# Kernel tuning notes

Measured on AMD Instinct MI355X. Metric: run time of the kernel, lower is better.

The kernel has to match this reference:

```python
import jax, jax.numpy as jnp
import numpy as np

NUM_ITERS = 20  # fixed in the original forward: transcribe(dna, iterations=20)


def transcribe(dna_seed, dna_a, dna_b):
    """Fractal DNA decompression: 20 elementwise contractive-map iterations
    over the full weight tensor, starting from the DNA seed."""
    def step(w, ab):
        a, b = ab
        w = a * w + b * jnp.sin(w)
        return w, None
    w, _ = jax.lax.scan(step, dna_seed, (dna_a, dna_b))
    return w  # [out_features, in_features]


def setup_inputs() -> dict:
    key = jax.random.key(0)
    k1, k2, k3, k4, k5 = jax.random.split(key, 5)
    TOKENS, IN_F, OUT_F = 2048, 4096, 4096
    return {
        "x": jax.random.normal(k1, (TOKENS, IN_F), dtype=jnp.float32),
        "dna_seed": jax.random.normal(k2, (OUT_F, IN_F), dtype=jnp.float32),
        "dna_a": jax.random.uniform(k3, (NUM_ITERS,), dtype=jnp.float32),
        "dna_b": jax.random.uniform(k4, (NUM_ITERS,), dtype=jnp.float32),
        "bias": jax.random.normal(k5, (OUT_F,), dtype=jnp.float32),
    }


def reference(x, dna_seed, dna_a, dna_b, bias):
    weight = transcribe(dna_seed, dna_a, dna_b)          # [out, in]
    # F.linear(x, weight, bias) == x @ weight.T + bias
    return jnp.einsum('ti,oi->to', x, weight) + bias     # [tokens, out]
```

## Files before the change

### kernel.cpp

```cpp
#include <hip/hip_runtime.h>

typedef __attribute__((ext_vector_type(8))) short short8;
typedef __attribute__((ext_vector_type(4))) float floatx4;

#define TOKENS 2048
#define IN_F   4096
#define OUT_F  4096
#define NITER  20

#define INV_2PI 0.15915494309189535f
#define TWO_PI  6.283185307179586f

__device__ __forceinline__ unsigned short f2bf(float f) {
    unsigned int u = __builtin_bit_cast(unsigned int, f);
    u += 0x7fffu + ((u >> 16) & 1u);
    return (unsigned short)(u >> 16);
}

__device__ __forceinline__ void step4(float4& v, float a, float bc) {
    v.x = __builtin_fmaf(bc, __builtin_amdgcn_sinf(v.x), a * v.x);
    v.y = __builtin_fmaf(bc, __builtin_amdgcn_sinf(v.y), a * v.y);
    v.z = __builtin_fmaf(bc, __builtin_amdgcn_sinf(v.z), a * v.z);
    v.w = __builtin_fmaf(bc, __builtin_amdgcn_sinf(v.w), a * v.w);
}

#define WBLOCKS (OUT_F * IN_F / 8 / 256)
#define XBLOCKS (TOKENS * IN_F / 8 / 256)

__global__ __launch_bounds__(256) void transcribe_fused_kernel(
    const float4* __restrict__ seed, const float4* __restrict__ xin,
    const float* __restrict__ da, const float* __restrict__ db,
    short8* __restrict__ w_out, short8* __restrict__ x_out)
{
    const int b = blockIdx.x;
    short8 o;
    if (b < WBLOCKS) {
        int i = b * 256 + threadIdx.x;
        float4 u = seed[2 * i];
        float4 v = seed[2 * i + 1];
        u.x *= INV_2PI; u.y *= INV_2PI; u.z *= INV_2PI; u.w *= INV_2PI;
        v.x *= INV_2PI; v.y *= INV_2PI; v.z *= INV_2PI; v.w *= INV_2PI;
#pragma unroll
        for (int t = 0; t < NITER; t++) {
            float a = da[t], bc = db[t] * INV_2PI;
            step4(u, a, bc);
            step4(v, a, bc);
        }
        o[0] = (short)f2bf(u.x * TWO_PI); o[1] = (short)f2bf(u.y * TWO_PI);
        o[2] = (short)f2bf(u.z * TWO_PI); o[3] = (short)f2bf(u.w * TWO_PI);
        o[4] = (short)f2bf(v.x * TWO_PI); o[5] = (short)f2bf(v.y * TWO_PI);
        o[6] = (short)f2bf(v.z * TWO_PI); o[7] = (short)f2bf(v.w * TWO_PI);
        w_out[i] = o;
    } else {
        int i = (b - WBLOCKS) * 256 + threadIdx.x;
        float4 u = xin[2 * i];
        float4 v = xin[2 * i + 1];
        o[0] = (short)f2bf(u.x); o[1] = (short)f2bf(u.y);
        o[2] = (short)f2bf(u.z); o[3] = (short)f2bf(u.w);
        o[4] = (short)f2bf(v.x); o[5] = (short)f2bf(v.y);
        o[6] = (short)f2bf(v.z); o[7] = (short)f2bf(v.w);
        x_out[i] = o;
    }
}

__device__ __forceinline__ void g2l16(const ushort* g, ushort* l) {
    __builtin_amdgcn_global_load_lds(
        (const __attribute__((address_space(1))) unsigned int*)g,
        (__attribute__((address_space(3))) unsigned int*)l, 16, 0, 0);
}

#define BK     64
#define BM     256
#define BN     128
#define NT     (IN_F / BK)
#define ASLOT  (BM * BK)
#define BSLOT  (BN * BK)
#define LDS_BYTES (3 * (ASLOT + BSLOT) * 2)

__global__ __launch_bounds__(512, 2) void gemm_bt_kernel(
    const ushort* __restrict__ A,
    const ushort* __restrict__ B,
    const float* __restrict__ bias,
    float* __restrict__ C)
{
    extern __shared__ ushort lds[];
    ushort* As = lds;
    ushort* Bs = lds + 3 * ASLOT;

    const int tid  = threadIdx.x;
    const int lane = tid & 63;
    const int wid  = tid >> 6;
    const int g    = wid >> 2;
    const int w2   = wid & 3;
    const int wm   = (w2 >> 1) << 7;
    const int wn   = (w2 & 1) << 6;
    const int fm   = lane & 15;
    const int q    = lane >> 4;

    const int bid = blockIdx.x;
    const int jj  = bid >> 3;
    const int bn  = (bid & 7) * 4 + (jj & 3);
    const int bm  = jj >> 2;

    const int gcol = (((lane & 7) ^ (lane >> 3)) << 3);

    const ushort* gA = A + (size_t)(bm * BM) * IN_F;
    const ushort* gB = B + (size_t)(bn * BN) * IN_F;

    floatx4 acc[8][4];
#pragma unroll
    for (int i = 0; i < 8; i++)
#pragma unroll
        for (int j = 0; j < 4; j++)
            acc[i][j] = (floatx4){0.f, 0.f, 0.f, 0.f};

#define STAGE(k0v, sl)                                                        \
    {                                                                         \
        _Pragma("unroll")                                                     \
        for (int u = 0; u < 4; u++) {                                         \
            const int cb = ((u << 3) | wid) << 6;                             \
            const int r  = (cb >> 3) + (lane >> 3);                           \
            g2l16(gA + (size_t)r * IN_F + (k0v) + gcol,                       \
                  As + (sl) * ASLOT + cb * 8 + lane * 8);                     \
        }                                                                     \
        _Pragma("unroll")                                                     \
        for (int u = 0; u < 2; u++) {                                         \
            const int cb = ((u << 3) | wid) << 6;                             \
            const int r  = (cb >> 3) + (lane >> 3);                           \
            g2l16(gB + (size_t)r * IN_F + (k0v) + gcol,                       \
                  Bs + (sl) * BSLOT + cb * 8 + lane * 8);                     \
        }                                                                     \
    }

#define LOADFRAG(sl)                                                          \
    const int sa = (((q + 4 * g) & 7) ^ (fm & 7)) << 3;                       \
    _Pragma("unroll")                                                         \
    for (int i = 0; i < 8; i++)                                               \
        af[i] = *(const short8*)(As + (sl) * ASLOT + (wm + i * 16 + fm) * BK + sa); \
    _Pragma("unroll")                                                         \
    for (int j = 0; j < 4; j++)                                               \
        bf[j] = *(const short8*)(Bs + (sl) * BSLOT + (wn + j * 16 + fm) * BK + sa);

#define MFMA32()                                                              \
    __builtin_amdgcn_s_setprio(1);                                            \
    _Pragma("unroll")                                                         \
    for (int i = 0; i < 8; i++)                                               \
        _Pragma("unroll")                                                     \
        for (int j = 0; j < 4; j++)                                           \
            acc[i][j] = __builtin_amdgcn_mfma_f32_16x16x32_bf16(              \
                af[i], bf[j], acc[i][j], 0, 0, 0);                            \
    __builtin_amdgcn_s_setprio(0);

#define TILE_MAIN(vm, sl, k3)                                                 \
    {                                                                         \
        asm volatile("s_waitcnt vmcnt(" #vm ")" ::: "memory");                \
        __builtin_amdgcn_s_barrier();                                         \
        short8 af[8], bf[4];                                                  \
        LOADFRAG(sl);                                                         \
        asm volatile("s_waitcnt lgkmcnt(0)" ::: "memory");                    \
        __builtin_amdgcn_s_barrier();                                         \
        STAGE(k3, sl);                                                        \
        __builtin_amdgcn_sched_barrier(0);                                    \
        MFMA32();                                                             \
    }

#define TILE_TAIL(vm, sl)                                                     \
    {                                                                         \
        asm volatile("s_waitcnt vmcnt(" #vm ")" ::: "memory");                \
        __builtin_amdgcn_s_barrier();                                         \
        short8 af[8], bf[4];                                                  \
        LOADFRAG(sl);                                                         \
        MFMA32();                                                             \
    }

    STAGE(0 * BK, 0);
    STAGE(1 * BK, 1);
    STAGE(2 * BK, 2);

    int st   = 0;
    int kpre = 3 * BK;
#pragma unroll 1
    for (int t = 0; t <= NT - 4; ++t) {
        TILE_MAIN(12, st, kpre);
        kpre += BK;
        st = (st == 2) ? 0 : st + 1;
    }
    TILE_TAIL(12, 1);
    TILE_TAIL(6, 2);
    TILE_TAIL(0, 0);

#undef STAGE
#undef LOADFRAG
#undef MFMA32
#undef TILE_MAIN
#undef TILE_TAIL

    __syncthreads();
    floatx4* red = (floatx4*)lds;
    if (g == 1) {
#pragma unroll
        for (int i = 0; i < 8; i++)
#pragma unroll
            for (int j = 0; j < 4; j++)
                red[(size_t)(w2 * 32 + i * 4 + j) * 64 + lane] = acc[i][j];
    }
    __syncthreads();
    if (g == 0) {
        const int cn = lane & 15;
        const int cm = (lane >> 4) << 2;
        float bv[4];
#pragma unroll
        for (int j = 0; j < 4; j++)
            bv[j] = bias[bn * BN + wn + j * 16 + cn];
#pragma unroll
        for (int i = 0; i < 8; i++) {
#pragma unroll
            for (int j = 0; j < 4; j++) {
                floatx4 p = red[(size_t)(w2 * 32 + i * 4 + j) * 64 + lane];
#pragma unroll
                for (int r = 0; r < 4; r++) acc[i][j][r] += p[r];
            }
#pragma unroll
            for (int r = 0; r < 4; r++) {
                int m = bm * BM + wm + i * 16 + cm + r;
                float* crow = C + (size_t)m * OUT_F + bn * BN + wn + cn;
#pragma unroll
                for (int j = 0; j < 4; j++)
                    crow[j * 16] = acc[i][j][r] + bv[j];
            }
        }
    }
}

extern "C" void kernel_launch(void* const* d_in, const int* in_sizes, int n_in,
                              void* d_out, int out_size, void* d_ws, size_t ws_size,
                              hipStream_t stream) {
    const float* x    = (const float*)d_in[0];
    const float* seed = (const float*)d_in[1];
    const float* da   = (const float*)d_in[2];
    const float* db   = (const float*)d_in[3];
    const float* bias = (const float*)d_in[4];
    float* out        = (float*)d_out;

    ushort* w_bf = (ushort*)d_ws;
    ushort* x_bf = w_bf + (size_t)OUT_F * IN_F;

    static bool lds_attr_set = false;
    if (!lds_attr_set) {
        hipFuncSetAttribute(reinterpret_cast<const void*>(gemm_bt_kernel),
                            hipFuncAttributeMaxDynamicSharedMemorySize,
                            LDS_BYTES);
        lds_attr_set = true;
    }

    transcribe_fused_kernel<<<WBLOCKS + XBLOCKS, 256, 0, stream>>>(
        (const float4*)seed, (const float4*)x, da, db,
        (short8*)w_bf, (short8*)x_bf);

    gemm_bt_kernel<<<dim3(32 * 8), dim3(512), LDS_BYTES, stream>>>(
        x_bf, w_bf, bias, out);
}
```

Measured before the change: 216.6 us.

## Software-pipeline LDS fragment loads with MFMA sub-phases in GEMM main loop

Splits each K-tile's 32 MFMAs into four sub-phases of eight and double-buffers the A and B fragment registers. The next sub-phase's LDS reads are issued while the current MFMAs run, and the next tile's fragments are prefetched across the tile boundary. The aim is to hide LDS read latency behind matrix-core work instead of stalling on lgkmcnt before each tile. The cost is extra VGPRs for the duplicate fragment buffers, which may lower occupancy, and a more intricate ordering of waits and barriers.

Result: no change. 214.1 us (-1.2%).

```diff
diff --git a/kernel.cpp b/kernel.cpp
--- a/kernel.cpp
+++ b/kernel.cpp
@@ -107,12 +107,19 @@
     const ushort* gA = A + (size_t)(bm * BM) * IN_F;
     const ushort* gB = B + (size_t)(bn * BN) * IN_F;
 
+    const int sa = (((q + 4 * g) & 7) ^ (fm & 7)) << 3;
+    const ushort* Abase = As + (wm + fm) * BK + sa;
+    const ushort* Bbase = Bs + (wn + fm) * BK + sa;
+
     floatx4 acc[8][4];
 #pragma unroll
     for (int i = 0; i < 8; i++)
 #pragma unroll
         for (int j = 0; j < 4; j++)
             acc[i][j] = (floatx4){0.f, 0.f, 0.f, 0.f};
+
+    short8 bf[4], bfn[4];
+    short8 afc[2], afn[2];
 
 #define STAGE(k0v, sl)                                                        \
     {                                                                         \
@@ -132,68 +139,89 @@
         }                                                                     \
     }
 
-#define LOADFRAG(sl)                                                          \
-    const int sa = (((q + 4 * g) & 7) ^ (fm & 7)) << 3;                       \
-    _Pragma("unroll")                                                         \
-    for (int i = 0; i < 8; i++)                                               \
-        af[i] = *(const short8*)(As + (sl) * ASLOT + (wm + i * 16 + fm) * BK + sa); \
+#define LOADA2(p_, sl)                                                        \
+    afn[0] = *(const short8*)(Abase + (sl) * ASLOT + (2 * (p_)    ) * (16 * BK)); \
+    afn[1] = *(const short8*)(Abase + (sl) * ASLOT + (2 * (p_) + 1) * (16 * BK));
+
+#define LOADB4(sl)                                                            \
     _Pragma("unroll")                                                         \
     for (int j = 0; j < 4; j++)                                               \
-        bf[j] = *(const short8*)(Bs + (sl) * BSLOT + (wn + j * 16 + fm) * BK + sa);
-
-#define MFMA32()                                                              \
+        bfn[j] = *(const short8*)(Bbase + (sl) * BSLOT + j * (16 * BK));
+
+#define MFMA8(p_)                                                             \
     __builtin_amdgcn_s_setprio(1);                                            \
     _Pragma("unroll")                                                         \
-    for (int i = 0; i < 8; i++)                                               \
+    for (int r = 0; r < 2; r++)                                               \
         _Pragma("unroll")                                                     \
         for (int j = 0; j < 4; j++)                                           \
-            acc[i][j] = __builtin_amdgcn_mfma_f32_16x16x32_bf16(              \
-                af[i], bf[j], acc[i][j], 0, 0, 0);                            \
+            acc[2 * (p_) + r][j] = __builtin_amdgcn_mfma_f32_16x16x32_bf16(   \
+                afc[r], bf[j], acc[2 * (p_) + r][j], 0, 0, 0);                \
     __builtin_amdgcn_s_setprio(0);
 
-#define TILE_MAIN(vm, sl, k3)                                                 \
+#define SUBPH(p_, sl)                                                         \
     {                                                                         \
-        asm volatile("s_waitcnt vmcnt(" #vm ")" ::: "memory");                \
-        __builtin_amdgcn_s_barrier();                                         \
-        short8 af[8], bf[4];                                                  \
-        LOADFRAG(sl);                                                         \
-        asm volatile("s_waitcnt lgkmcnt(0)" ::: "memory");                    \
-        __builtin_amdgcn_s_barrier();                                         \
-        STAGE(k3, sl);                                                        \
+        LOADA2((p_) + 1, sl);                                                 \
         __builtin_amdgcn_sched_barrier(0);                                    \
-        MFMA32();                                                             \
-    }
-
-#define TILE_TAIL(vm, sl)                                                     \
-    {                                                                         \
-        asm volatile("s_waitcnt vmcnt(" #vm ")" ::: "memory");                \
-        __builtin_amdgcn_s_barrier();                                         \
-        short8 af[8], bf[4];                                                  \
-        LOADFRAG(sl);                                                         \
-        MFMA32();                                                             \
-    }
+        MFMA8(p_);                                                            \
+        afc[0] = afn[0]; afc[1] = afn[1];                                     \
+    }
+
+#define COPY_NEXT()                                                           \
+    bf[0] = bfn[0]; bf[1] = bfn[1]; bf[2] = bfn[2]; bf[3] = bfn[3];           \
+    afc[0] = afn[0]; afc[1] = afn[1];
 
     STAGE(0 * BK, 0);
     STAGE(1 * BK, 1);
     STAGE(2 * BK, 2);
+    asm volatile("s_waitcnt vmcnt(12)" ::: "memory");
+    __builtin_amdgcn_s_barrier();
+    LOADB4(0); LOADA2(0, 0);
+    __builtin_amdgcn_sched_barrier(0);
+    COPY_NEXT();
 
     int st   = 0;
     int kpre = 3 * BK;
 #pragma unroll 1
     for (int t = 0; t <= NT - 4; ++t) {
-        TILE_MAIN(12, st, kpre);
+        const int stn = (st == 2) ? 0 : st + 1;
+        SUBPH(0, st);
+        SUBPH(1, st);
+        SUBPH(2, st);
+        asm volatile("s_waitcnt lgkmcnt(0)" ::: "memory");
+        __builtin_amdgcn_s_barrier();
+        STAGE(kpre, st);
+        asm volatile("s_waitcnt vmcnt(12)" ::: "memory");
+        __builtin_amdgcn_s_barrier();
+        LOADB4(stn); LOADA2(0, stn);
+        __builtin_amdgcn_sched_barrier(0);
+        MFMA8(3);
+        COPY_NEXT();
+        st = stn;
         kpre += BK;
-        st = (st == 2) ? 0 : st + 1;
-    }
-    TILE_TAIL(12, 1);
-    TILE_TAIL(6, 2);
-    TILE_TAIL(0, 0);
+    }
+    SUBPH(0, 1); SUBPH(1, 1); SUBPH(2, 1);
+    asm volatile("s_waitcnt vmcnt(6)" ::: "memory");
+    __builtin_amdgcn_s_barrier();
+    LOADB4(2); LOADA2(0, 2);
+    __builtin_amdgcn_sched_barrier(0);
+    MFMA8(3);
+    COPY_NEXT();
+    SUBPH(0, 2); SUBPH(1, 2); SUBPH(2, 2);
+    asm volatile("s_waitcnt vmcnt(0)" ::: "memory");
+    __builtin_amdgcn_s_barrier();
+    LOADB4(0); LOADA2(0, 0);
+    __builtin_amdgcn_sched_barrier(0);
+    MFMA8(3);
+    COPY_NEXT();
+    SUBPH(0, 0); SUBPH(1, 0); SUBPH(2, 0);
+    MFMA8(3);
 
 #undef STAGE
-#undef LOADFRAG
-#undef MFMA32
-#undef TILE_MAIN
-#undef TILE_TAIL
+#undef LOADA2
+#undef LOADB4
+#undef MFMA8
+#undef SUBPH
+#undef COPY_NEXT
 
     __syncthreads();
     floatx4* red = (floatx4*)lds;
```
